# Optimization experiments

Measured on AMD Instinct MI355X. Metric: run time of the kernel, lower is better.

## Reference

```python
import jax, jax.numpy as jnp
import numpy as np


def setup_inputs() -> dict:
    key = jax.random.key(0)
    k1, k2, k3, k4 = jax.random.split(key, 4)
    B = 1048576        # batch of annotator ids
    A = 65536          # num_annotators
    D = 8              # latent_dims
    annotator = jax.random.randint(k1, (B,), 0, A, dtype=jnp.int64)
    posterior_mu = jax.random.normal(k2, (A, D), dtype=jnp.float32)
    posterior_covtril = jax.random.normal(k3, (A, D, D), dtype=jnp.float32)
    eps = jax.random.normal(k4, (B, D), dtype=jnp.float32)
    return {
        "annotator": annotator,
        "posterior_mu": posterior_mu,
        "posterior_covtril": posterior_covtril,
        "eps": eps,
    }


def reference(annotator, posterior_mu, posterior_covtril, eps):
    # Batched equivalent of the per-annotator MVN rsample loop:
    #   z_i = mu[a_i] + tril(covtril[a_i]) @ eps_i
    mu = posterior_mu[annotator]                 # [B, D]   gather
    L = jnp.tril(posterior_covtril[annotator])   # [B, D, D] gather + tril mask
    z = mu + jnp.einsum("bij,bj->bi", L, eps)    # reparameterized sample
    return z
```

## Files before the change

### kernel.cpp

```cpp
#include <hip/hip_runtime.h>
#include <hip/hip_bf16.h>
#include <hip/hip_fp16.h>


typedef float    f32x4 __attribute__((ext_vector_type(4)));
typedef _Float16 f16x8 __attribute__((ext_vector_type(8)));

__device__ __constant__ const int SL_SRC[28] = {
    8,
    16,17,
    24,25,26,
    32,33,34,35,
    40,41,42,43,44,
    48,49,50,51,52,53,
    56,57,58,59,60,61,62
};
__device__ __constant__ const int DIAG_SRC[8] = {0,9,18,27,36,45,54,63};

__global__ __launch_bounds__(256) void pack_kernel(
    const float* __restrict__ mu,
    const float* __restrict__ L,
    _Float16* __restrict__ sl,
    _Float16* __restrict__ md,
    int A)
{
    int a = blockIdx.x * blockDim.x + threadIdx.x;
    if (a >= A) return;

    const f32x4* muv = reinterpret_cast<const f32x4*>(mu + (size_t)a * 8);
    const f32x4* Lv  = reinterpret_cast<const f32x4*>(L + (size_t)a * 64);
    f32x4 m0 = __builtin_nontemporal_load(muv);
    f32x4 m1 = __builtin_nontemporal_load(muv + 1);
    f32x4 r[16];
    #pragma unroll
    for (int k = 0; k < 16; ++k) r[k] = __builtin_nontemporal_load(Lv + k);

    f16x8 slc[4];
    #pragma unroll
    for (int k = 0; k < 28; ++k) {
        const int f = SL_SRC[k];
        slc[k >> 3][k & 7] = (_Float16)r[f >> 2][f & 3];
    }
    #pragma unroll
    for (int k = 28; k < 32; ++k) slc[k >> 3][k & 7] = (_Float16)0.f;

    f16x8 md0, md1;
    #pragma unroll
    for (int j = 0; j < 4; ++j) { md0[j] = (_Float16)m0[j]; md0[4+j] = (_Float16)m1[j]; }
    #pragma unroll
    for (int j = 0; j < 8; ++j) {
        const int f = DIAG_SRC[j];
        md1[j] = (_Float16)r[f >> 2][f & 3];
    }

    f16x8* so = reinterpret_cast<f16x8*>(sl + (size_t)a * 32);
    #pragma unroll
    for (int c = 0; c < 4; ++c) __builtin_nontemporal_store(slc[c], so + c);
    f16x8* mo = reinterpret_cast<f16x8*>(md + (size_t)a * 16);
    __builtin_nontemporal_store(md0, mo);
    __builtin_nontemporal_store(md1, mo + 1);
}

__global__ __launch_bounds__(256) void lv_main(
    const int* __restrict__ ann,
    const _Float16* __restrict__ sl,
    const _Float16* __restrict__ md,
    const float* __restrict__ eps,
    float* __restrict__ out,
    int B)
{
    int b = blockIdx.x * blockDim.x + threadIdx.x;
    if (b >= B) return;

    const int a = __builtin_nontemporal_load(ann + b);

    const f32x4* epsv = reinterpret_cast<const f32x4*>(eps + (size_t)b * 8);
    const f32x4 e0 = __builtin_nontemporal_load(epsv);
    const f32x4 e1 = __builtin_nontemporal_load(epsv + 1);

    const f16x8* slp = reinterpret_cast<const f16x8*>(sl + (size_t)a * 32);
    const f16x8 c0 = slp[0], c1 = slp[1], c2 = slp[2], c3 = slp[3];
    const f16x8* mdp = reinterpret_cast<const f16x8*>(md + (size_t)a * 16);
    const f16x8 md0 = mdp[0], md1 = mdp[1];

    const float e[8] = {e0[0], e0[1], e0[2], e0[3], e1[0], e1[1], e1[2], e1[3]};

    float z[8];
    #pragma unroll
    for (int i = 0; i < 8; ++i) z[i] = (float)md0[i] + (float)md1[i] * e[i];

    const f16x8 slc[4] = {c0, c1, c2, c3};
    #pragma unroll
    for (int i = 1; i < 8; ++i) {
        const int base = i * (i - 1) / 2;
        #pragma unroll
        for (int j = 0; j < i; ++j) {
            const int s = base + j;
            z[i] += (float)slc[s >> 3][s & 7] * e[j];
        }
    }

    f32x4* outv = reinterpret_cast<f32x4*>(out + (size_t)b * 8);
    f32x4 o0 = {z[0], z[1], z[2], z[3]};
    f32x4 o1 = {z[4], z[5], z[6], z[7]};
    __builtin_nontemporal_store(o0, outv);
    __builtin_nontemporal_store(o1, outv + 1);
}

__global__ __launch_bounds__(256) void lv_kernel_f32(
    const int* __restrict__ ann,
    const float* __restrict__ mu,
    const float* __restrict__ L,
    const float* __restrict__ eps,
    float* __restrict__ out,
    int B)
{
    int b = blockIdx.x * blockDim.x + threadIdx.x;
    if (b >= B) return;
    const int a = ann[b];
    const f32x4* epsv = reinterpret_cast<const f32x4*>(eps + (size_t)b * 8);
    const f32x4 e0 = epsv[0];
    const f32x4 e1 = epsv[1];
    const float e[8] = {e0[0], e0[1], e0[2], e0[3], e1[0], e1[1], e1[2], e1[3]};
    const f32x4* muv = reinterpret_cast<const f32x4*>(mu + (size_t)a * 8);
    const f32x4 m0 = muv[0];
    const f32x4 m1 = muv[1];
    float z[8] = {m0[0], m0[1], m0[2], m0[3], m1[0], m1[1], m1[2], m1[3]};
    const f32x4* Lv = reinterpret_cast<const f32x4*>(L + (size_t)a * 64);
    #pragma unroll
    for (int i = 0; i < 4; ++i) {
        const f32x4 r0 = Lv[i * 2];
        #pragma unroll
        for (int j = 0; j <= i; ++j) z[i] += r0[j] * e[j];
    }
    #pragma unroll
    for (int i = 4; i < 8; ++i) {
        const f32x4 r0 = Lv[i * 2];
        const f32x4 r1 = Lv[i * 2 + 1];
        const float rr[8] = {r0[0], r0[1], r0[2], r0[3], r1[0], r1[1], r1[2], r1[3]};
        #pragma unroll
        for (int j = 0; j <= i; ++j) z[i] += rr[j] * e[j];
    }
    f32x4* outv = reinterpret_cast<f32x4*>(out + (size_t)b * 8);
    f32x4 o0 = {z[0], z[1], z[2], z[3]};
    f32x4 o1 = {z[4], z[5], z[6], z[7]};
    outv[0] = o0;
    outv[1] = o1;
}

extern "C" void kernel_launch(void* const* d_in, const int* in_sizes, int n_in,
                              void* d_out, int out_size, void* d_ws, size_t ws_size,
                              hipStream_t stream) {
    const int*   ann = (const int*)d_in[0];
    const float* mu  = (const float*)d_in[1];
    const float* L   = (const float*)d_in[2];
    const float* eps = (const float*)d_in[3];
    float* out = (float*)d_out;

    const int B = in_sizes[0];
    const int A = in_sizes[1] / 8;

    const size_t sl_bytes = (size_t)A * 32 * sizeof(_Float16);
    const size_t md_bytes = (size_t)A * 16 * sizeof(_Float16);
    if (ws_size >= sl_bytes + md_bytes) {
        _Float16* sl = (_Float16*)d_ws;
        _Float16* md = (_Float16*)((char*)d_ws + sl_bytes);
        pack_kernel<<<(A + 255) / 256, 256, 0, stream>>>(mu, L, sl, md, A);
        lv_main<<<(B + 255) / 256, 256, 0, stream>>>(ann, sl, md, eps, out, B);
    } else {
        lv_kernel_f32<<<(B + 255) / 256, 256, 0, stream>>>(ann, mu, L, eps, out, B);
    }
}
```

Measured before the change: 51.58 us.

## Merge packed tables into one 96-byte record and process four rows per thread

The packed fp16 strict-lower, mean and diagonal values now sit in a single interleaved 96-byte record per annotator instead of two separate tables, so each gathered row touches one contiguous region rather than two. The main kernel also handles four batch rows per thread, issuing all index, record and eps loads before any compute to raise memory-level parallelism. The cost is more registers per thread and a quarter as many blocks. The record is padded from 88 to 96 bytes, and the index load plus dependent gather still sit on the critical path.

```diff
diff --git a/kernel.cpp b/kernel.cpp
--- a/kernel.cpp
+++ b/kernel.cpp
@@ -7,21 +7,15 @@
 typedef _Float16 f16x8 __attribute__((ext_vector_type(8)));
 
 __device__ __constant__ const int SL_SRC[28] = {
-    8,
-    16,17,
-    24,25,26,
-    32,33,34,35,
-    40,41,42,43,44,
-    48,49,50,51,52,53,
-    56,57,58,59,60,61,62
+    8, 16,17, 24,25,26, 32,33,34,35, 40,41,42,43,44,
+    48,49,50,51,52,53, 56,57,58,59,60,61,62
 };
 __device__ __constant__ const int DIAG_SRC[8] = {0,9,18,27,36,45,54,63};
 
 __global__ __launch_bounds__(256) void pack_kernel(
     const float* __restrict__ mu,
     const float* __restrict__ L,
-    _Float16* __restrict__ sl,
-    _Float16* __restrict__ md,
+    _Float16* __restrict__ rec,
     int A)
 {
     int a = blockIdx.x * blockDim.x + threadIdx.x;
@@ -35,76 +29,96 @@
     #pragma unroll
     for (int k = 0; k < 16; ++k) r[k] = __builtin_nontemporal_load(Lv + k);
 
-    f16x8 slc[4];
+    f16x8 ch[6];
     #pragma unroll
     for (int k = 0; k < 28; ++k) {
         const int f = SL_SRC[k];
-        slc[k >> 3][k & 7] = (_Float16)r[f >> 2][f & 3];
+        ch[k >> 3][k & 7] = (_Float16)r[f >> 2][f & 3];
     }
     #pragma unroll
-    for (int k = 28; k < 32; ++k) slc[k >> 3][k & 7] = (_Float16)0.f;
+    for (int i = 0; i < 8; ++i) {
+        const int k = 28 + i;
+        const float v = (i < 4) ? m0[i] : m1[i - 4];
+        ch[k >> 3][k & 7] = (_Float16)v;
+    }
+    #pragma unroll
+    for (int i = 0; i < 8; ++i) {
+        const int k = 36 + i;
+        const int f = DIAG_SRC[i];
+        ch[k >> 3][k & 7] = (_Float16)r[f >> 2][f & 3];
+    }
+    #pragma unroll
+    for (int k = 44; k < 48; ++k) ch[k >> 3][k & 7] = (_Float16)0.f;
 
-    f16x8 md0, md1;
+    f16x8* o = reinterpret_cast<f16x8*>(rec + (size_t)a * 48);
     #pragma unroll
-    for (int j = 0; j < 4; ++j) { md0[j] = (_Float16)m0[j]; md0[4+j] = (_Float16)m1[j]; }
-    #pragma unroll
-    for (int j = 0; j < 8; ++j) {
-        const int f = DIAG_SRC[j];
-        md1[j] = (_Float16)r[f >> 2][f & 3];
-    }
+    for (int c = 0; c < 6; ++c) __builtin_nontemporal_store(ch[c], o + c);
+}
 
-    f16x8* so = reinterpret_cast<f16x8*>(sl + (size_t)a * 32);
-    #pragma unroll
-    for (int c = 0; c < 4; ++c) __builtin_nontemporal_store(slc[c], so + c);
-    f16x8* mo = reinterpret_cast<f16x8*>(md + (size_t)a * 16);
-    __builtin_nontemporal_store(md0, mo);
-    __builtin_nontemporal_store(md1, mo + 1);
-}
+#define ROWS 4
 
 __global__ __launch_bounds__(256) void lv_main(
     const int* __restrict__ ann,
-    const _Float16* __restrict__ sl,
-    const _Float16* __restrict__ md,
+    const _Float16* __restrict__ rec,
     const float* __restrict__ eps,
     float* __restrict__ out,
     int B)
 {
-    int b = blockIdx.x * blockDim.x + threadIdx.x;
-    if (b >= B) return;
+    const int tid = threadIdx.x;
+    const long base = (long)blockIdx.x * (256 * ROWS);
 
-    const int a = __builtin_nontemporal_load(ann + b);
-
-    const f32x4* epsv = reinterpret_cast<const f32x4*>(eps + (size_t)b * 8);
-    const f32x4 e0 = __builtin_nontemporal_load(epsv);
-    const f32x4 e1 = __builtin_nontemporal_load(epsv + 1);
-
-    const f16x8* slp = reinterpret_cast<const f16x8*>(sl + (size_t)a * 32);
-    const f16x8 c0 = slp[0], c1 = slp[1], c2 = slp[2], c3 = slp[3];
-    const f16x8* mdp = reinterpret_cast<const f16x8*>(md + (size_t)a * 16);
-    const f16x8 md0 = mdp[0], md1 = mdp[1];
-
-    const float e[8] = {e0[0], e0[1], e0[2], e0[3], e1[0], e1[1], e1[2], e1[3]};
-
-    float z[8];
+    long row[ROWS];
+    int a[ROWS];
     #pragma unroll
-    for (int i = 0; i < 8; ++i) z[i] = (float)md0[i] + (float)md1[i] * e[i];
-
-    const f16x8 slc[4] = {c0, c1, c2, c3};
-    #pragma unroll
-    for (int i = 1; i < 8; ++i) {
-        const int base = i * (i - 1) / 2;
-        #pragma unroll
-        for (int j = 0; j < i; ++j) {
-            const int s = base + j;
-            z[i] += (float)slc[s >> 3][s & 7] * e[j];
-        }
+    for (int k = 0; k < ROWS; ++k) {
+        row[k] = base + k * 256 + tid;
+        a[k] = (row[k] < (long)B) ? __builtin_nontemporal_load(ann + row[k]) : 0;
     }
 
-    f32x4* outv = reinterpret_cast<f32x4*>(out + (size_t)b * 8);
-    f32x4 o0 = {z[0], z[1], z[2], z[3]};
-    f32x4 o1 = {z[4], z[5], z[6], z[7]};
-    __builtin_nontemporal_store(o0, outv);
-    __builtin_nontemporal_store(o1, outv + 1);
+    f16x8 ch[ROWS][6];
+    #pragma unroll
+    for (int k = 0; k < ROWS; ++k) {
+        const f16x8* rp = reinterpret_cast<const f16x8*>(rec + (size_t)a[k] * 48);
+        #pragma unroll
+        for (int c = 0; c < 6; ++c) ch[k][c] = rp[c];
+    }
+
+    f32x4 ev0[ROWS], ev1[ROWS];
+    #pragma unroll
+    for (int k = 0; k < ROWS; ++k) {
+        const long rc = (row[k] < (long)B) ? row[k] : 0;
+        const f32x4* ep = reinterpret_cast<const f32x4*>(eps + (size_t)rc * 8);
+        ev0[k] = __builtin_nontemporal_load(ep);
+        ev1[k] = __builtin_nontemporal_load(ep + 1);
+    }
+
+    #pragma unroll
+    for (int k = 0; k < ROWS; ++k) {
+        if (row[k] >= (long)B) continue;
+        const float e[8] = {ev0[k][0], ev0[k][1], ev0[k][2], ev0[k][3],
+                            ev1[k][0], ev1[k][1], ev1[k][2], ev1[k][3]};
+        float z[8];
+        #pragma unroll
+        for (int i = 0; i < 8; ++i) {
+            const int km = 28 + i, kd = 36 + i;
+            z[i] = (float)ch[k][km >> 3][km & 7]
+                 + (float)ch[k][kd >> 3][kd & 7] * e[i];
+        }
+        #pragma unroll
+        for (int i = 1; i < 8; ++i) {
+            const int sb = i * (i - 1) / 2;
+            #pragma unroll
+            for (int j = 0; j < i; ++j) {
+                const int s = sb + j;
+                z[i] += (float)ch[k][s >> 3][s & 7] * e[j];
+            }
+        }
+        f32x4* outv = reinterpret_cast<f32x4*>(out + (size_t)row[k] * 8);
+        f32x4 o0 = {z[0], z[1], z[2], z[3]};
+        f32x4 o1 = {z[4], z[5], z[6], z[7]};
+        __builtin_nontemporal_store(o0, outv);
+        __builtin_nontemporal_store(o1, outv + 1);
+    }
 }
 
 __global__ __launch_bounds__(256) void lv_kernel_f32(
@@ -160,13 +174,13 @@
     const int B = in_sizes[0];
     const int A = in_sizes[1] / 8;
 
-    const size_t sl_bytes = (size_t)A * 32 * sizeof(_Float16);
-    const size_t md_bytes = (size_t)A * 16 * sizeof(_Float16);
-    if (ws_size >= sl_bytes + md_bytes) {
-        _Float16* sl = (_Float16*)d_ws;
-        _Float16* md = (_Float16*)((char*)d_ws + sl_bytes);
-        pack_kernel<<<(A + 255) / 256, 256, 0, stream>>>(mu, L, sl, md, A);
-        lv_main<<<(B + 255) / 256, 256, 0, stream>>>(ann, sl, md, eps, out, B);
+    const size_t rec_bytes = (size_t)A * 48 * sizeof(_Float16);
+    if (ws_size >= rec_bytes) {
+        _Float16* rec = (_Float16*)d_ws;
+        pack_kernel<<<(A + 255) / 256, 256, 0, stream>>>(mu, L, rec, A);
+        const int rows_per_block = 256 * ROWS;
+        const int blocks = (B + rows_per_block - 1) / rows_per_block;
+        lv_main<<<blocks, 256, 0, stream>>>(ann, rec, eps, out, B);
     } else {
         lv_kernel_f32<<<(B + 255) / 256, 256, 0, stream>>>(ann, mu, L, eps, out, B);
     }
```

After: 50.01 us. 1.03x faster.
